# Performance work log

Hardware: AMD Instinct MI355X
Metric: run time of the kernel (lower is better)

The kernel has to match this reference:

```python
import jax, jax.numpy as jnp
import numpy as np
from jax.scipy.special import logsumexp

B, S, H, L = 64, 512, 1024, 9  # batch, seq_len, hidden_size, num_labels


def setup_inputs() -> dict:
    key = jax.random.key(0)
    ks = jax.random.split(key, 6)
    inputs = jax.random.normal(ks[0], (B, S, H), jnp.float32)
    labels = jax.random.randint(ks[1], (B, S), 0, L).astype(jnp.int64)
    mask = jnp.ones((B, S), jnp.int32)
    # fc parameters (nn.Linear(hidden_size, num_labels))
    W = jax.random.normal(ks[2], (L, H), jnp.float32) / np.sqrt(H)
    b = jnp.zeros((L,), jnp.float32)
    # CRF parameters (include_start_end_trans=True)
    trans_m = jax.random.normal(ks[3], (L, L), jnp.float32) * 0.1
    start_scores = jax.random.normal(ks[4], (L,), jnp.float32) * 0.1
    end_scores = jax.random.normal(ks[5], (L,), jnp.float32) * 0.1
    return dict(inputs=inputs, labels=labels, mask=mask, W=W, b=b,
                trans_m=trans_m, start_scores=start_scores, end_scores=end_scores)


def _crf_nll_mean(inputs, W, b, trans_m, start_scores, end_scores, labels, mask):
    # logits = fc(inputs): [B, S, L]
    logits = jnp.einsum('bsh,lh->bsl', inputs, W) + b
    feats = jnp.swapaxes(logits, 0, 1)           # [S, B, L] (fastNLP transposes)
    tags = jnp.swapaxes(labels, 0, 1)            # [S, B]
    m = jnp.swapaxes(mask, 0, 1).astype(feats.dtype)  # [S, B]
    seq_len, batch, n_tags = feats.shape

    # ---- log-partition via forward algorithm (lax.scan over time) ----
    alpha0 = feats[0] + start_scores[None, :]    # [B, L]

    def step(alpha, x):
        emit, mt = x                              # emit: [B, L], mt: [B]
        # tmp[b, i, j] = alpha[b, i] + trans_m[i, j] + emit[b, j]
        tmp = alpha[:, :, None] + trans_m[None, :, :] + emit[:, None, :]
        new = logsumexp(tmp, axis=1)              # [B, L]
        alpha = jnp.where(mt[:, None] > 0, new, alpha)
        return alpha, None

    alpha, _ = jax.lax.scan(step, alpha0, (feats[1:], m[1:]))
    norm = logsumexp(alpha + end_scores[None, :], axis=1)   # [B]

    # ---- gold path score ----
    emit = jnp.take_along_axis(feats, tags[:, :, None], axis=2)[:, :, 0] * m  # [S, B]
    trans = trans_m[tags[:-1], tags[1:]] * m[1:]                               # [S-1, B]
    score = emit.sum(0) + trans.sum(0)                                         # [B]
    last_idx = m.sum(0).astype(jnp.int32) - 1                                  # [B]
    last_tags = tags[last_idx, jnp.arange(batch)]
    score = score + start_scores[tags[0]] + end_scores[last_tags]

    # loss = crf(logits, labels, mask).mean()
    return jnp.mean(norm - score)


def reference(inputs, labels, mask, W, b, trans_m, start_scores, end_scores):
    return _crf_nll_mean(inputs, W, b, trans_m, start_scores, end_scores, labels, mask)
```

## Files before the change

### kernel.cpp

```cpp
#include <hip/hip_runtime.h>


#define BATCH 64
#define SEQ   512
#define HID   1024
#define NLAB  9
#define CHUNK 32
#define NCHUNK (SEQ / CHUNK)
#define RPB   64

__device__ __forceinline__ float exp2_fast(float x) { return __builtin_amdgcn_exp2f(x); }
__device__ __forceinline__ float log2_fast(float x) { return __builtin_amdgcn_logf(x); }

#define LOG2E 1.4426950408889634f
#define LN2   0.6931471805599453f

__global__ __launch_bounds__(256) void logits_chunk_kernel(
    const float* __restrict__ inp, const float* __restrict__ Wg,
    const float* __restrict__ bias, const float* __restrict__ trans,
    const int* __restrict__ mask, float* __restrict__ feats,
    float* __restrict__ P, float* __restrict__ out)
{
    if (blockIdx.x == 0 && threadIdx.x == 0) out[0] = 0.0f;

    __shared__ float Wl[NLAB * HID];
    __shared__ float femit[RPB][NLAB];
    const int tid = threadIdx.x;
    #pragma unroll
    for (int i = 0; i < 9; ++i)
        ((float4*)Wl)[tid + i * 256] = ((const float4*)Wg)[tid + i * 256];
    __syncthreads();

    const int lane = tid & 63;
    const int wv   = tid >> 6;
    const int p    = lane & 15;
    const int q    = lane >> 4;
    const int grp  = wv * 4 + q;
    const int lrow0 = grp * 4;
    const long grow0 = (long)blockIdx.x * RPB + lrow0;
    const float* rb = inp + grow0 * HID + p * 4;
    const float* wb = Wl + p * 4;

    float acc[4][NLAB];
    #pragma unroll
    for (int r = 0; r < 4; ++r)
        #pragma unroll
        for (int l = 0; l < NLAB; ++l) acc[r][l] = 0.0f;

    #pragma unroll 1
    for (int cc = 0; cc < 8; ++cc) {
        const int off = cc * 128;
        float4 xs[4][2];
        #pragma unroll
        for (int r = 0; r < 4; ++r) {
            xs[r][0] = *(const float4*)(rb + r * HID + off);
            xs[r][1] = *(const float4*)(rb + r * HID + off + 64);
        }
        #pragma unroll
        for (int l = 0; l < NLAB; ++l) {
            const float* w = wb + l * HID + off;
            float4 w0 = *(const float4*)(w);
            float4 w1 = *(const float4*)(w + 64);
            #pragma unroll
            for (int r = 0; r < 4; ++r) {
                float a = acc[r][l];
                a = fmaf(xs[r][0].x, w0.x, a);
                a = fmaf(xs[r][0].y, w0.y, a);
                a = fmaf(xs[r][0].z, w0.z, a);
                a = fmaf(xs[r][0].w, w0.w, a);
                a = fmaf(xs[r][1].x, w1.x, a);
                a = fmaf(xs[r][1].y, w1.y, a);
                a = fmaf(xs[r][1].z, w1.z, a);
                a = fmaf(xs[r][1].w, w1.w, a);
                acc[r][l] = a;
            }
        }
    }

    #pragma unroll
    for (int r = 0; r < 4; ++r) {
        #pragma unroll
        for (int l = 0; l < NLAB; ++l) {
            float a = acc[r][l];
            a += __shfl_xor(a, 8, 64);
            a += __shfl_xor(a, 4, 64);
            a += __shfl_xor(a, 2, 64);
            a += __shfl_xor(a, 1, 64);
            acc[r][l] = a;
        }
    }
    if (p == 0) {
        #pragma unroll
        for (int r = 0; r < 4; ++r) {
            float* o = feats + (grow0 + r) * NLAB;
            #pragma unroll
            for (int l = 0; l < NLAB; ++l) {
                float f = (acc[r][l] + bias[l]) * LOG2E;
                o[l] = f;  femit[lrow0 + r][l] = f;
            }
        }
    }
    __syncthreads();

    const int half = wv >> 1;
    const int sub  = wv & 1;
    const int b = blockIdx.x >> 3;
    const int c = ((blockIdx.x & 7) << 1) | half;
    const int crow0 = half * CHUNK;

    int g = lane / 9;
    const int jj = lane - g * 9;
    bool act = sub ? (g < 2) : (g < 7);
    int i = act ? (sub * 7 + g) : 0;
    const int sbase = g * 9;

    float tr[NLAB];
    #pragma unroll
    for (int k = 0; k < NLAB; ++k) tr[k] = trans[k * NLAB + jj] * LOG2E;
    const float tri = trans[i * NLAB + jj] * LOG2E;

    const int* mb = mask + b * SEQ + c * CHUNK;
    const int ts = (c == 0) ? 1 : 0;

    float a;
    {
        int m0 = mb[ts];
        float e0 = femit[crow0 + ts][jj];
        float aid = (i == jj) ? 0.0f : -1e30f;
        a = (m0 > 0) ? (tri + e0) : aid;
    }

    int m_nxt = mb[ts + 1];
    for (int t = ts + 1; t < CHUNK; ++t) {
        float e = femit[crow0 + t][jj];
        int  mt = m_nxt;
        if (t + 1 < CHUNK) m_nxt = mb[t + 1];
        float v[NLAB];
        #pragma unroll
        for (int k = 0; k < NLAB; ++k) v[k] = __shfl(a, sbase + k, 64) + tr[k];
        float m01 = fmaxf(v[0], v[1]), m23 = fmaxf(v[2], v[3]);
        float m45 = fmaxf(v[4], v[5]), m67 = fmaxf(v[6], v[7]);
        float mx = fmaxf(fmaxf(fmaxf(m01, m23), fmaxf(m45, m67)), v[8]);
        float s = 0.0f;
        #pragma unroll
        for (int k = 0; k < NLAB; ++k) s += exp2_fast(v[k] - mx);
        float an = mx + log2_fast(s) + e;
        a = (mt > 0) ? an : a;
    }
    if (act)
        P[(long)(b * NCHUNK + c) * 81 + i * NLAB + jj] = a;
}

__global__ __launch_bounds__(64) void final_kernel(
    const float* __restrict__ feats, const float* __restrict__ trans,
    const float* __restrict__ startv, const float* __restrict__ endv,
    const int* __restrict__ labels, const int* __restrict__ mask,
    const float* __restrict__ P, float* __restrict__ out)
{
    const int b = blockIdx.x, lane = threadIdx.x;
    const float* fb = feats + (long)b * SEQ * NLAB;
    const int* lb = labels + b * SEQ;
    const int* mb = mask + b * SEQ;

    float gsum = 0.0f; int msum = 0;
    for (int t = lane; t < SEQ; t += 64) {
        int tag = lb[t];
        int mt = mb[t];
        if (mt > 0) {
            gsum += fb[t * NLAB + tag];
            msum++;
            if (t > 0) gsum += trans[lb[t - 1] * NLAB + tag] * LOG2E;
        }
    }
    #pragma unroll
    for (int off = 32; off > 0; off >>= 1) {
        gsum += __shfl_xor(gsum, off, 64);
        msum += __shfl_xor(msum, off, 64);
    }

    const int j = lane % 9;
    float al = fb[j] + startv[j] * LOG2E;
    const float* Pb = P + (long)b * NCHUNK * 81;
    float pc[NLAB];
    #pragma unroll
    for (int i = 0; i < NLAB; ++i) pc[i] = Pb[i * NLAB + j];
    #pragma unroll
    for (int c = 0; c < NCHUNK; ++c) {
        float pn[NLAB];
        if (c < NCHUNK - 1) {
            #pragma unroll
            for (int i = 0; i < NLAB; ++i) pn[i] = Pb[(c + 1) * 81 + i * NLAB + j];
        } else {
            #pragma unroll
            for (int i = 0; i < NLAB; ++i) pn[i] = 0.0f;
        }
        float v[NLAB];
        #pragma unroll
        for (int i = 0; i < NLAB; ++i) v[i] = __shfl(al, i, 64) + pc[i];
        float m01 = fmaxf(v[0], v[1]), m23 = fmaxf(v[2], v[3]);
        float m45 = fmaxf(v[4], v[5]), m67 = fmaxf(v[6], v[7]);
        float mx = fmaxf(fmaxf(fmaxf(m01, m23), fmaxf(m45, m67)), v[8]);
        float s = 0.0f;
        #pragma unroll
        for (int i = 0; i < NLAB; ++i) s += exp2_fast(v[i] - mx);
        al = mx + log2_fast(s);
        #pragma unroll
        for (int i = 0; i < NLAB; ++i) pc[i] = pn[i];
    }
    al += endv[j] * LOG2E;

    float v[NLAB];
    #pragma unroll
    for (int i = 0; i < NLAB; ++i) v[i] = __shfl(al, i, 64);
    float m01 = fmaxf(v[0], v[1]), m23 = fmaxf(v[2], v[3]);
    float m45 = fmaxf(v[4], v[5]), m67 = fmaxf(v[6], v[7]);
    float mx = fmaxf(fmaxf(fmaxf(m01, m23), fmaxf(m45, m67)), v[8]);
    float s = 0.0f;
    #pragma unroll
    for (int i = 0; i < NLAB; ++i) s += exp2_fast(v[i] - mx);
    float norm = mx + log2_fast(s);

    if (lane == 0) {
        int li = (msum > 0) ? (msum - 1) : 0;
        float score = gsum + startv[lb[0]] * LOG2E + endv[lb[li]] * LOG2E;
        atomicAdd(out, (norm - score) * (LN2 / (float)BATCH));
    }
}

extern "C" void kernel_launch(void* const* d_in, const int* in_sizes, int n_in,
                              void* d_out, int out_size, void* d_ws, size_t ws_size,
                              hipStream_t stream)
{
    const float* inp    = (const float*)d_in[0];
    const int*   labels = (const int*)d_in[1];
    const int*   mask   = (const int*)d_in[2];
    const float* W      = (const float*)d_in[3];
    const float* bias   = (const float*)d_in[4];
    const float* trans  = (const float*)d_in[5];
    const float* startv = (const float*)d_in[6];
    const float* endv   = (const float*)d_in[7];

    float* feats = (float*)d_ws;
    float* P     = feats + BATCH * SEQ * NLAB;
    float* out   = (float*)d_out;

    hipLaunchKernelGGL(logits_chunk_kernel, dim3(BATCH * SEQ / RPB), dim3(256), 0,
                       stream, inp, W, bias, trans, mask, feats, P, out);
    hipLaunchKernelGGL(final_kernel, dim3(BATCH), dim3(64), 0, stream,
                       feats, trans, startv, endv, labels, mask, P, out);
}
```

Measured before the change: 235.1 us.

## Halve rows per block and double-buffer input loads in logits GEMV

```diff
diff --git a/kernel.cpp b/kernel.cpp
--- a/kernel.cpp
+++ b/kernel.cpp
@@ -7,13 +7,40 @@
 #define NLAB  9
 #define CHUNK 32
 #define NCHUNK (SEQ / CHUNK)
-#define RPB   64
+#define RPB   32
 
 __device__ __forceinline__ float exp2_fast(float x) { return __builtin_amdgcn_exp2f(x); }
 __device__ __forceinline__ float log2_fast(float x) { return __builtin_amdgcn_logf(x); }
 
 #define LOG2E 1.4426950408889634f
 #define LN2   0.6931471805599453f
+
+#define LOADX(X, OFF)                                              \
+    {   X[0][0] = *(const float4*)(rb + (OFF));                    \
+        X[0][1] = *(const float4*)(rb + (OFF) + 64);               \
+        X[1][0] = *(const float4*)(rb + HID + (OFF));              \
+        X[1][1] = *(const float4*)(rb + HID + (OFF) + 64); }
+
+#define FMAX(X, OFF)                                               \
+    _Pragma("unroll")                                              \
+    for (int l = 0; l < NLAB; ++l) {                               \
+        const float* w = wb + l * HID + (OFF);                     \
+        float4 w0 = *(const float4*)(w);                           \
+        float4 w1 = *(const float4*)(w + 64);                      \
+        _Pragma("unroll")                                          \
+        for (int r = 0; r < 2; ++r) {                              \
+            float a = acc[r][l];                                   \
+            a = fmaf(X[r][0].x, w0.x, a);                          \
+            a = fmaf(X[r][0].y, w0.y, a);                          \
+            a = fmaf(X[r][0].z, w0.z, a);                          \
+            a = fmaf(X[r][0].w, w0.w, a);                          \
+            a = fmaf(X[r][1].x, w1.x, a);                          \
+            a = fmaf(X[r][1].y, w1.y, a);                          \
+            a = fmaf(X[r][1].z, w1.z, a);                          \
+            a = fmaf(X[r][1].w, w1.w, a);                          \
+            acc[r][l] = a;                                         \
+        }                                                          \
+    }
 
 __global__ __launch_bounds__(256) void logits_chunk_kernel(
     const float* __restrict__ inp, const float* __restrict__ Wg,
@@ -36,49 +63,30 @@
     const int p    = lane & 15;
     const int q    = lane >> 4;
     const int grp  = wv * 4 + q;
-    const int lrow0 = grp * 4;
+    const int lrow0 = grp * 2;
     const long grow0 = (long)blockIdx.x * RPB + lrow0;
     const float* rb = inp + grow0 * HID + p * 4;
     const float* wb = Wl + p * 4;
 
-    float acc[4][NLAB];
-    #pragma unroll
-    for (int r = 0; r < 4; ++r)
+    float acc[2][NLAB];
+    #pragma unroll
+    for (int r = 0; r < 2; ++r)
         #pragma unroll
         for (int l = 0; l < NLAB; ++l) acc[r][l] = 0.0f;
 
+    float4 xsA[2][2], xsB[2][2];
+    LOADX(xsA, 0);
     #pragma unroll 1
-    for (int cc = 0; cc < 8; ++cc) {
-        const int off = cc * 128;
-        float4 xs[4][2];
-        #pragma unroll
-        for (int r = 0; r < 4; ++r) {
-            xs[r][0] = *(const float4*)(rb + r * HID + off);
-            xs[r][1] = *(const float4*)(rb + r * HID + off + 64);
-        }
-        #pragma unroll
-        for (int l = 0; l < NLAB; ++l) {
-            const float* w = wb + l * HID + off;
-            float4 w0 = *(const float4*)(w);
-            float4 w1 = *(const float4*)(w + 64);
-            #pragma unroll
-            for (int r = 0; r < 4; ++r) {
-                float a = acc[r][l];
-                a = fmaf(xs[r][0].x, w0.x, a);
-                a = fmaf(xs[r][0].y, w0.y, a);
-                a = fmaf(xs[r][0].z, w0.z, a);
-                a = fmaf(xs[r][0].w, w0.w, a);
-                a = fmaf(xs[r][1].x, w1.x, a);
-                a = fmaf(xs[r][1].y, w1.y, a);
-                a = fmaf(xs[r][1].z, w1.z, a);
-                a = fmaf(xs[r][1].w, w1.w, a);
-                acc[r][l] = a;
-            }
-        }
-    }
-
-    #pragma unroll
-    for (int r = 0; r < 4; ++r) {
+    for (int ccp = 0; ccp < 4; ++ccp) {
+        const int offA = ccp * 256;
+        LOADX(xsB, offA + 128);
+        FMAX(xsA, offA);
+        if (ccp < 3) LOADX(xsA, offA + 256);
+        FMAX(xsB, offA + 128);
+    }
+
+    #pragma unroll
+    for (int r = 0; r < 2; ++r) {
         #pragma unroll
         for (int l = 0; l < NLAB; ++l) {
             float a = acc[r][l];
@@ -91,7 +99,7 @@
     }
     if (p == 0) {
         #pragma unroll
-        for (int r = 0; r < 4; ++r) {
+        for (int r = 0; r < 2; ++r) {
             float* o = feats + (grow0 + r) * NLAB;
             #pragma unroll
             for (int l = 0; l < NLAB; ++l) {
@@ -102,16 +110,15 @@
     }
     __syncthreads();
 
-    const int half = wv >> 1;
-    const int sub  = wv & 1;
-    const int b = blockIdx.x >> 3;
-    const int c = ((blockIdx.x & 7) << 1) | half;
-    const int crow0 = half * CHUNK;
+    if (wv >= 2) return;
+
+    const int b = blockIdx.x >> 4;
+    const int c = blockIdx.x & (NCHUNK - 1);
 
     int g = lane / 9;
     const int jj = lane - g * 9;
-    bool act = sub ? (g < 2) : (g < 7);
-    int i = act ? (sub * 7 + g) : 0;
+    bool act = (wv == 0) ? (g < 7) : (g < 2);
+    int i = act ? (wv * 7 + g) : 0;
     const int sbase = g * 9;
 
     float tr[NLAB];
@@ -125,14 +132,14 @@
     float a;
     {
         int m0 = mb[ts];
-        float e0 = femit[crow0 + ts][jj];
+        float e0 = femit[ts][jj];
         float aid = (i == jj) ? 0.0f : -1e30f;
         a = (m0 > 0) ? (tri + e0) : aid;
     }
 
     int m_nxt = mb[ts + 1];
     for (int t = ts + 1; t < CHUNK; ++t) {
-        float e = femit[crow0 + t][jj];
+        float e = femit[t][jj];
         int  mt = m_nxt;
         if (t + 1 < CHUNK) m_nxt = mb[t + 1];
         float v[NLAB];
```

Result: no change. 232.6 us (-1.1%).
